# Optimization experiments

Measured on AMD Instinct MI355X. Metric: run time of the kernel, lower is better.

The kernel has to match this reference:

```python
import jax, jax.numpy as jnp
import numpy as np

L = 4000      # num identities
C = 8         # num cameras; center bank is label-major: center j -> (label j//C, cam j%C)
T = 0.07      # temperature
HARD_NEG_K = 50
LAMDA = 0.5


def setup_inputs() -> dict:
    key = jax.random.key(0)
    k1, k2, k3, k4 = jax.random.split(key, 4)
    n, d = 256, 2048
    feats = jax.random.normal(k1, (n, d), dtype=jnp.float32)
    centers = jax.random.normal(k2, (L * C, d), dtype=jnp.float32)
    centers = centers / jnp.linalg.norm(centers, axis=1, keepdims=True)  # bank is kept unit-norm
    labels = jax.random.randint(k3, (n,), 0, L, dtype=jnp.int64)
    camids = jax.random.randint(k4, (n,), 0, C, dtype=jnp.int64)
    return {"feats": feats, "centers": centers, "labels": labels, "camids": camids, "epoch": 5}


def _cap_losses(feats, centers, labels, camids):
    n = feats.shape[0]
    M = centers.shape[0]
    feats = feats / jnp.linalg.norm(feats, axis=1, keepdims=True)  # F.normalize(p=2, dim=1)
    center_labels = jnp.arange(M) // C
    center_cams = jnp.arange(M) % C

    sims = jnp.einsum('nd,md->nm', feats, centers) / T  # [n, M] scaled similarities
    own_idx = labels * C + camids                        # cam_label_index[(label, cam)]
    own = sims[jnp.arange(n), own_idx]                   # numerator logits
    exp_sims = jnp.exp(sims)                             # unit vectors => sims <= 1/T ~ 14.3, safe

    # ---- intra-camera loss: denominator over centers sharing the sample's camid ----
    cam_mask = (center_cams[None, :] == camids[:, None])
    denom_intra = jnp.sum(exp_sims * cam_mask, axis=1)
    loss_i = own - jnp.log(denom_intra)                  # log(frac_up/frac_down)
    # mean per camid, then sum over camids present in the batch, negated
    ones = jnp.ones((n,), dtype=feats.dtype)
    cam_sums = jax.ops.segment_sum(loss_i, camids, num_segments=C)
    cam_cnts = jax.ops.segment_sum(ones, camids, num_segments=C)
    loss_intra = -jnp.sum(jnp.where(cam_cnts > 0, cam_sums / jnp.maximum(cam_cnts, 1.0), 0.0))

    # ---- inter loss: same-label centers + first-K hard negatives (in bank order) ----
    lbl_mask = (center_labels[None, :] == labels[:, None])
    other = ~lbl_mask
    # torch concatenates other-label centers in label order and takes the FIRST 50 (a slice,
    # not top-k); label-major bank order makes that = first 50 other-label centers by index.
    rank = jnp.cumsum(other.astype(jnp.int32), axis=1)
    hard_mask = other & (rank <= HARD_NEG_K)
    denom_inter = jnp.sum(exp_sims * lbl_mask, axis=1) + jnp.sum(exp_sims * hard_mask, axis=1)
    loss_j = own - jnp.log(denom_inter)
    lbl_sums = jax.ops.segment_sum(loss_j, labels, num_segments=L)
    lbl_cnts = jax.ops.segment_sum(ones, labels, num_segments=L)
    loss_inter = -jnp.sum(jnp.where(lbl_cnts > 0, lbl_sums / jnp.maximum(lbl_cnts, 1.0), 0.0))

    return loss_intra, loss_inter


def reference(feats, centers, labels, camids, epoch):
    loss_intra, loss_inter = _cap_losses(feats, centers, labels, camids)
    if epoch < 5:  # epoch is a static python int
        return loss_intra
    return jnp.stack([loss_intra, LAMDA * loss_inter])
```

## Files before the change

kernel.cpp:

```cpp
#include <hip/hip_runtime.h>

typedef __attribute__((ext_vector_type(8))) __bf16 bf16x8;
typedef __attribute__((ext_vector_type(4))) __bf16 bf16x4;
typedef __attribute__((ext_vector_type(4))) float f32x4;

#define N_SAMP 256
#define DIM    2048
#define NCENT  32000
#define INV_T  14.285714285714285714f
#define NWG    250
#define NSTEP  32

__global__ __launch_bounds__(256) void norm_kernel(const float* __restrict__ feats,
                                                   __bf16* __restrict__ fnorm,
                                                   float* __restrict__ d_acc) {
    int row = blockIdx.x;
    int tid = threadIdx.x;
    if (row < 16) d_acc[row * 256 + tid] = 0.f;
    const float* src = feats + (size_t)row * DIM;
    float4 v0 = reinterpret_cast<const float4*>(src)[2 * tid];
    float4 v1 = reinterpret_cast<const float4*>(src)[2 * tid + 1];
    float ss = v0.x * v0.x + v0.y * v0.y + v0.z * v0.z + v0.w * v0.w
             + v1.x * v1.x + v1.y * v1.y + v1.z * v1.z + v1.w * v1.w;
    #pragma unroll
    for (int off = 1; off < 64; off <<= 1) ss += __shfl_xor(ss, off, 64);
    __shared__ float wsum[4];
    if ((tid & 63) == 0) wsum[tid >> 6] = ss;
    __syncthreads();
    float inv = 1.0f / sqrtf(wsum[0] + wsum[1] + wsum[2] + wsum[3]);
    bf16x8 o;
    o[0] = (__bf16)(v0.x * inv); o[1] = (__bf16)(v0.y * inv);
    o[2] = (__bf16)(v0.z * inv); o[3] = (__bf16)(v0.w * inv);
    o[4] = (__bf16)(v1.x * inv); o[5] = (__bf16)(v1.y * inv);
    o[6] = (__bf16)(v1.z * inv); o[7] = (__bf16)(v1.w * inv);
    *reinterpret_cast<bf16x8*>(fnorm + (size_t)row * DIM + tid * 8) = o;
}

__global__ __launch_bounds__(512, 2) void sims_kernel(
    const __bf16* __restrict__ fnorm, const float* __restrict__ centers,
    const int* __restrict__ labels, const int* __restrict__ camids,
    float* __restrict__ d_acc, float* __restrict__ d_own)
{
    __shared__ __align__(16) char sA[2][32768];
    __shared__ __align__(16) char sB[2][16384];

    const int tid  = threadIdx.x;
    const int wave = tid >> 6;
    const int lane = tid & 63;
    const int l15  = lane & 15;
    const int lhi  = lane >> 4;

    const int nb    = blockIdx.x;
    const int cbase = nb * 128;

    const int wr = (wave >> 1) * 64;
    const int wc = (wave & 1) * 64;

    f32x4 acc[4][4] = {};

    const float4* bsrc = reinterpret_cast<const float4*>(centers);
    const uint4*  asrc = reinterpret_cast<const uint4*>(fnorm);

    const int arow = tid >> 1, ah = tid & 1;
    const int brow = tid >> 2, bq = tid & 3;

    auto issue = [&](int step, uint4 (&a)[4], float4 (&b)[4]) {
        #pragma unroll
        for (int q = 0; q < 4; ++q)
            a[q] = asrc[(size_t)arow * 256 + step * 8 + ah * 4 + q];
        #pragma unroll
        for (int q = 0; q < 4; ++q)
            b[q] = bsrc[(size_t)(cbase + brow) * 512 + step * 16 + bq * 4 + q];
    };
    auto wrbuf = [&](int buf, const uint4 (&a)[4], const float4 (&b)[4]) {
        #pragma unroll
        for (int q = 0; q < 4; ++q) {
            int lin = arow * 128 + ah * 64 + q * 16;
            int adr = lin ^ ((arow & 7) << 4);
            *reinterpret_cast<uint4*>(&sA[buf][adr]) = a[q];
        }
        #pragma unroll
        for (int q = 0; q < 4; ++q) {
            bf16x4 o;
            o[0] = (__bf16)b[q].x; o[1] = (__bf16)b[q].y;
            o[2] = (__bf16)b[q].z; o[3] = (__bf16)b[q].w;
            int lin = brow * 128 + bq * 32 + q * 8;
            int adr = lin ^ ((brow & 7) << 4);
            *reinterpret_cast<uint2*>(&sB[buf][adr]) = __builtin_bit_cast(uint2, o);
        }
    };
    auto compute_half = [&](int buf, int h) {
        bf16x8 af[4], bf[4];
        #pragma unroll
        for (int mi = 0; mi < 4; ++mi) {
            int row = wr + mi * 16 + l15;
            int adr = (row * 128 + h * 64 + lhi * 16) ^ ((row & 7) << 4);
            af[mi] = *reinterpret_cast<const bf16x8*>(&sA[buf][adr]);
        }
        #pragma unroll
        for (int ni = 0; ni < 4; ++ni) {
            int row = wc + ni * 16 + l15;
            int adr = (row * 128 + h * 64 + lhi * 16) ^ ((row & 7) << 4);
            bf[ni] = *reinterpret_cast<const bf16x8*>(&sB[buf][adr]);
        }
        #pragma unroll
        for (int mi = 0; mi < 4; ++mi)
            #pragma unroll
            for (int ni = 0; ni < 4; ++ni)
                acc[mi][ni] = __builtin_amdgcn_mfma_f32_16x16x32_bf16(
                    af[mi], bf[ni], acc[mi][ni], 0, 0, 0);
    };
    #define BAR() do { asm volatile("s_waitcnt lgkmcnt(0)" ::: "memory"); \
                       __builtin_amdgcn_s_barrier(); } while (0)

    uint4  aSA[4], aSB[4];
    float4 bSA[4], bSB[4];

    issue(0, aSA, bSA);
    issue(1, aSB, bSB);
    wrbuf(0, aSA, bSA);
    BAR();
    for (int t = 0; t < NSTEP; t += 2) {
        if (t + 2 < NSTEP) issue(t + 2, aSA, bSA);
        compute_half(0, 0);
        compute_half(0, 1);
        wrbuf(1, aSB, bSB);
        BAR();
        if (t + 3 < NSTEP) issue(t + 3, aSB, bSB);
        compute_half(1, 0);
        compute_half(1, 1);
        if (t + 2 < NSTEP) {
            wrbuf(0, aSA, bSA);
            BAR();
        }
    }

    float* slot = d_acc + (nb & 7) * 512;
    #pragma unroll
    for (int mi = 0; mi < 4; ++mi) {
        #pragma unroll
        for (int r = 0; r < 4; ++r) {
            int i   = wr + mi * 16 + lhi * 4 + r;
            int lab = labels[i], cam = camids[i];
            int oidx = lab * 8 + cam;
            float pi = 0.f, pj = 0.f;
            #pragma unroll
            for (int ni = 0; ni < 4; ++ni) {
                int c = cbase + wc + ni * 16 + l15;
                float s = acc[mi][ni][r] * INV_T;
                float e = __expf(s);
                if ((l15 & 7) == cam) pi += e;
                bool ol = ((c >> 3) == lab);
                bool hard = (!ol) && (c < ((c < lab * 8) ? 50 : 58));
                if (ol || hard) pj += e;
                if (c == oidx) d_own[i] = s;
            }
            #pragma unroll
            for (int off = 1; off < 16; off <<= 1) {
                pi += __shfl_xor(pi, off, 64);
                pj += __shfl_xor(pj, off, 64);
            }
            if (l15 == 0) {
                atomicAdd(&slot[i], pi);
                atomicAdd(&slot[N_SAMP + i], pj);
            }
        }
    }
}

__global__ __launch_bounds__(256) void finalize_kernel(
    const float* __restrict__ d_acc, const float* __restrict__ d_own,
    const int* __restrict__ labels, const int* __restrict__ camids,
    float* __restrict__ out, int out_size)
{
    __shared__ int s_lab[N_SAMP], s_cam[N_SAMP];
    __shared__ float wsum[8];
    int tid = threadIdx.x;
    s_lab[tid] = labels[tid];
    s_cam[tid] = camids[tid];
    __syncthreads();
    int myl = s_lab[tid], myc = s_cam[tid];
    int nl = 0, nc = 0;
    for (int j = 0; j < N_SAMP; ++j) {
        nl += (s_lab[j] == myl);
        nc += (s_cam[j] == myc);
    }
    float di = 0.f, dj = 0.f;
    #pragma unroll
    for (int s = 0; s < 8; ++s) {
        di += d_acc[s * 512 + tid];
        dj += d_acc[s * 512 + 256 + tid];
    }
    float own = d_own[tid];
    float li = own - logf(di);
    float lj = own - logf(dj);
    float a = li / (float)nc;
    float b = lj / (float)nl;
    #pragma unroll
    for (int off = 1; off < 64; off <<= 1) {
        a += __shfl_xor(a, off, 64);
        b += __shfl_xor(b, off, 64);
    }
    if ((tid & 63) == 0) { wsum[tid >> 6] = a; wsum[4 + (tid >> 6)] = b; }
    __syncthreads();
    if (tid == 0) {
        float sa = wsum[0] + wsum[1] + wsum[2] + wsum[3];
        float sb = wsum[4] + wsum[5] + wsum[6] + wsum[7];
        out[0] = -sa;
        if (out_size > 1) out[1] = -0.5f * sb;
    }
}

extern "C" void kernel_launch(void* const* d_in, const int* in_sizes, int n_in,
                              void* d_out, int out_size, void* d_ws, size_t ws_size,
                              hipStream_t stream) {
    const float* feats   = (const float*)d_in[0];
    const float* centers = (const float*)d_in[1];
    const int*   labels  = (const int*)d_in[2];
    const int*   camids  = (const int*)d_in[3];
    float* out = (float*)d_out;

    __bf16* fnorm = (__bf16*)d_ws;
    float* d_acc  = (float*)((char*)d_ws + (size_t)N_SAMP * DIM * sizeof(__bf16));
    float* d_own  = d_acc + 8 * 2 * N_SAMP;

    norm_kernel<<<N_SAMP, 256, 0, stream>>>(feats, fnorm, d_acc);
    sims_kernel<<<NWG, 512, 0, stream>>>(fnorm, centers, labels, camids, d_acc, d_own);
    finalize_kernel<<<1, 256, 0, stream>>>(d_acc, d_own, labels, camids, out, out_size);
}
```

Before: 96.37 us.

## Split sims tiles into 128x128 with 500 workgroups and XCD-aware mapping

Halves the per-workgroup tile to 128 samples by 128 centers with a 32-wide K step, doubling the grid to 500 workgroups of 256 threads. Block indices are remapped so both sample halves of the same center block land on the same XCD, aiming to share center reads in L2. This raises parallelism and occupancy but reads and converts each fp32 center tile twice, which may raise HBM traffic if L2 reuse fails.

```diff
diff --git a/kernel.cpp b/kernel.cpp
--- a/kernel.cpp
+++ b/kernel.cpp
@@ -8,8 +8,7 @@
 #define DIM    2048
 #define NCENT  32000
 #define INV_T  14.285714285714285714f
-#define NWG    250
-#define NSTEP  32
+#define NWG    500
 
 __global__ __launch_bounds__(256) void norm_kernel(const float* __restrict__ feats,
                                                    __bf16* __restrict__ fnorm,
@@ -36,13 +35,13 @@
     *reinterpret_cast<bf16x8*>(fnorm + (size_t)row * DIM + tid * 8) = o;
 }
 
-__global__ __launch_bounds__(512, 2) void sims_kernel(
+__global__ __launch_bounds__(256, 2) void sims_kernel(
     const __bf16* __restrict__ fnorm, const float* __restrict__ centers,
     const int* __restrict__ labels, const int* __restrict__ camids,
     float* __restrict__ d_acc, float* __restrict__ d_own)
 {
-    __shared__ __align__(16) char sA[2][32768];
-    __shared__ __align__(16) char sB[2][16384];
+    __shared__ __align__(16) char sA[2][8192];
+    __shared__ __align__(16) char sB[2][8192];
 
     const int tid  = threadIdx.x;
     const int wave = tid >> 6;
@@ -50,7 +49,11 @@
     const int l15  = lane & 15;
     const int lhi  = lane >> 4;
 
-    const int nb    = blockIdx.x;
+    const int d   = blockIdx.x;
+    const int xcd = d & 7, loc = d >> 3;
+    const int lid = (xcd < 4 ? xcd * 63 : 252 + (xcd - 4) * 62) + loc;
+    const int nb  = lid >> 1;
+    const int mb  = lid & 1;
     const int cbase = nb * 128;
 
     const int wr = (wave >> 1) * 64;
@@ -61,46 +64,51 @@
     const float4* bsrc = reinterpret_cast<const float4*>(centers);
     const uint4*  asrc = reinterpret_cast<const uint4*>(fnorm);
 
-    const int arow = tid >> 1, ah = tid & 1;
-    const int brow = tid >> 2, bq = tid & 3;
-
-    auto issue = [&](int step, uint4 (&a)[4], float4 (&b)[4]) {
-        #pragma unroll
-        for (int q = 0; q < 4; ++q)
-            a[q] = asrc[(size_t)arow * 256 + step * 8 + ah * 4 + q];
-        #pragma unroll
-        for (int q = 0; q < 4; ++q)
-            b[q] = bsrc[(size_t)(cbase + brow) * 512 + step * 16 + bq * 4 + q];
+    auto issue = [&](int step, float4 (&b)[4], uint4 (&a)[2]) {
+        #pragma unroll
+        for (int q = 0; q < 4; ++q) {
+            int f = q * 256 + tid;
+            int row = f >> 3, pos = f & 7;
+            b[q] = bsrc[(size_t)(cbase + row) * 512 + step * 8 + pos];
+        }
+        #pragma unroll
+        for (int q = 0; q < 2; ++q) {
+            int f = q * 256 + tid;
+            int row = f >> 2, pos = f & 3;
+            a[q] = asrc[(size_t)(mb * 128 + row) * 256 + step * 4 + pos];
+        }
     };
-    auto wrbuf = [&](int buf, const uint4 (&a)[4], const float4 (&b)[4]) {
+    auto wrbuf = [&](int buf, const float4 (&b)[4], const uint4 (&a)[2]) {
         #pragma unroll
         for (int q = 0; q < 4; ++q) {
-            int lin = arow * 128 + ah * 64 + q * 16;
-            int adr = lin ^ ((arow & 7) << 4);
-            *reinterpret_cast<uint4*>(&sA[buf][adr]) = a[q];
-        }
-        #pragma unroll
-        for (int q = 0; q < 4; ++q) {
+            int f = q * 256 + tid;
+            int row = f >> 3, pos = f & 7;
+            int adr = (row * 64 + pos * 8) ^ ((row & 7) << 4);
             bf16x4 o;
             o[0] = (__bf16)b[q].x; o[1] = (__bf16)b[q].y;
             o[2] = (__bf16)b[q].z; o[3] = (__bf16)b[q].w;
-            int lin = brow * 128 + bq * 32 + q * 8;
-            int adr = lin ^ ((brow & 7) << 4);
             *reinterpret_cast<uint2*>(&sB[buf][adr]) = __builtin_bit_cast(uint2, o);
         }
+        #pragma unroll
+        for (int q = 0; q < 2; ++q) {
+            int f = q * 256 + tid;
+            int row = f >> 2, pos = f & 3;
+            int adr = (row * 64 + pos * 16) ^ ((row & 7) << 4);
+            *reinterpret_cast<uint4*>(&sA[buf][adr]) = a[q];
+        }
     };
-    auto compute_half = [&](int buf, int h) {
+    auto compute = [&](int buf) {
         bf16x8 af[4], bf[4];
         #pragma unroll
         for (int mi = 0; mi < 4; ++mi) {
             int row = wr + mi * 16 + l15;
-            int adr = (row * 128 + h * 64 + lhi * 16) ^ ((row & 7) << 4);
+            int adr = (row * 64 + lhi * 16) ^ ((row & 7) << 4);
             af[mi] = *reinterpret_cast<const bf16x8*>(&sA[buf][adr]);
         }
         #pragma unroll
         for (int ni = 0; ni < 4; ++ni) {
             int row = wc + ni * 16 + l15;
-            int adr = (row * 128 + h * 64 + lhi * 16) ^ ((row & 7) << 4);
+            int adr = (row * 64 + lhi * 16) ^ ((row & 7) << 4);
             bf[ni] = *reinterpret_cast<const bf16x8*>(&sB[buf][adr]);
         }
         #pragma unroll
@@ -113,34 +121,32 @@
     #define BAR() do { asm volatile("s_waitcnt lgkmcnt(0)" ::: "memory"); \
                        __builtin_amdgcn_s_barrier(); } while (0)
 
-    uint4  aSA[4], aSB[4];
     float4 bSA[4], bSB[4];
-
-    issue(0, aSA, bSA);
-    issue(1, aSB, bSB);
-    wrbuf(0, aSA, bSA);
+    uint4  aSA[2], aSB[2];
+
+    issue(0, bSA, aSA);
+    issue(1, bSB, aSB);
+    wrbuf(0, bSA, aSA);
     BAR();
-    for (int t = 0; t < NSTEP; t += 2) {
-        if (t + 2 < NSTEP) issue(t + 2, aSA, bSA);
-        compute_half(0, 0);
-        compute_half(0, 1);
-        wrbuf(1, aSB, bSB);
+    for (int t = 0; t < 64; t += 2) {
+        if (t + 2 < 64) issue(t + 2, bSA, aSA);
+        compute(0);
+        wrbuf(1, bSB, aSB);
         BAR();
-        if (t + 3 < NSTEP) issue(t + 3, aSB, bSB);
-        compute_half(1, 0);
-        compute_half(1, 1);
-        if (t + 2 < NSTEP) {
-            wrbuf(0, aSA, bSA);
+        if (t + 3 < 64) issue(t + 3, bSB, aSB);
+        compute(1);
+        if (t + 2 < 64) {
+            wrbuf(0, bSA, aSA);
             BAR();
         }
     }
 
-    float* slot = d_acc + (nb & 7) * 512;
+    float* slot = d_acc + (d & 7) * 512;
     #pragma unroll
     for (int mi = 0; mi < 4; ++mi) {
         #pragma unroll
         for (int r = 0; r < 4; ++r) {
-            int i   = wr + mi * 16 + lhi * 4 + r;
+            int i   = mb * 128 + wr + mi * 16 + lhi * 4 + r;
             int lab = labels[i], cam = camids[i];
             int oidx = lab * 8 + cam;
             float pi = 0.f, pj = 0.f;
@@ -225,6 +231,6 @@
     float* d_own  = d_acc + 8 * 2 * N_SAMP;
 
     norm_kernel<<<N_SAMP, 256, 0, stream>>>(feats, fnorm, d_acc);
-    sims_kernel<<<NWG, 512, 0, stream>>>(fnorm, centers, labels, camids, d_acc, d_own);
+    sims_kernel<<<NWG, 256, 0, stream>>>(fnorm, centers, labels, camids, d_acc, d_own);
     finalize_kernel<<<1, 256, 0, stream>>>(d_acc, d_own, labels, camids, out, out_size);
 }
```

Result: slower. 152.8 us (+58.5%).
